# Performance work log

Measured on AMD Instinct MI355X. Metric: run time of the kernel, lower is better.

The kernel has to match this reference:

```python
import jax, jax.numpy as jnp
import numpy as np

BN_EPS = 1e-5

# Fixed shifted-difference kernels from the torch module (4,1,3,3)
_W1 = np.array([[[-1, 0, 0], [0, 1, 0], [0, 0, 0]],
                [[0, -1, 0], [0, 1, 0], [0, 0, 0]],
                [[0, 0, -1], [0, 1, 0], [0, 0, 0]],
                [[0, 0, 0], [-1, 1, 0], [0, 0, 0]]], dtype=np.float32).reshape(4, 1, 3, 3)
_W2 = np.ascontiguousarray(_W1[:, :, ::-1, ::-1])
SHIFTS = (1, 3)


def _conv(x, w, dilation=1):
    return jax.lax.conv_general_dilated(
        x, w, window_strides=(1, 1), padding='SAME',
        rhs_dilation=(dilation, dilation),
        dimension_numbers=('NCHW', 'OIHW', 'NCHW'))


def setup_inputs() -> dict:
    key = jax.random.key(0)
    ks = jax.random.split(key, 3)
    B, C, H, W = 4, 32, 512, 512
    cen = jax.random.normal(ks[0], (B, C, H, W), dtype=jnp.float32)
    w_conv = jax.random.normal(ks[1], (C, C, 3, 3), dtype=jnp.float32) * (1.0 / np.sqrt(9 * C))
    w_1x1 = jax.random.normal(ks[2], (1, C, 1, 1), dtype=jnp.float32) * (1.0 / np.sqrt(C))
    return {
        'cen': cen,
        'w_conv': w_conv,
        'bn_gamma': jnp.ones((C,), jnp.float32),
        'bn_beta': jnp.zeros((C,), jnp.float32),
        'bn_mean': jnp.zeros((C,), jnp.float32),
        'bn_var': jnp.ones((C,), jnp.float32),
        'w_1x1': w_1x1,
        'b_1x1': jnp.zeros((1,), jnp.float32),
    }


def reference(cen, w_conv, bn_gamma, bn_beta, bn_mean, bn_var, w_1x1, b_1x1):
    k1 = jnp.asarray(_W1)
    k2 = jnp.asarray(_W2)

    # down_conv: BaseConv(C->C, k3, s1) = Conv(no bias) + BN(eval) + SiLU, then 1x1 conv C->1
    x = _conv(cen, w_conv)
    inv = bn_gamma / jnp.sqrt(bn_var + BN_EPS)
    x = x * inv[None, :, None, None] + (bn_beta - bn_mean * inv)[None, :, None, None]
    x = jax.nn.silu(x)
    x = _conv(x, w_1x1) + b_1x1[None, :, None, None]  # [B,1,H,W]

    # circ_shift per dilation: fixed diff convs, product, min over 4 directions
    outs = []
    for s in SHIFTS:
        o1 = _conv(x, k1, dilation=s)  # [B,4,H,W]
        o2 = _conv(x, k2, dilation=s)
        outs.append(jnp.min(o1 * o2, axis=1, keepdims=True))  # [B,1,H,W]
    outs = jnp.stack(outs, axis=-1)  # [B,1,H,W,n_shifts]

    att = (jnp.max(outs, axis=-1) + jnp.mean(outs, axis=-1)) * 0.5
    att = jax.nn.sigmoid(jax.nn.relu(att))  # [B,1,H,W]
    return cen * att
```

## Files before the change

kernel.cpp:

```cpp
#include <hip/hip_runtime.h>
#include <hip/hip_bf16.h>
#include <math.h>

typedef __attribute__((ext_vector_type(8))) short bf16x8;
typedef __attribute__((ext_vector_type(4))) float f32x4;

#define HH 512
#define WW 512
#define CC 32

__device__ __forceinline__ unsigned short f2bf(float f) {
    unsigned u = __float_as_uint(f);
    u = (u + 0x7fffu + ((u >> 16) & 1u)) >> 16;
    return (unsigned short)u;
}

__global__ __launch_bounds__(256) void prepack(const float* __restrict__ wconv,
                                               unsigned short* __restrict__ wbuf) {
    int e = blockIdx.x * 256 + threadIdx.x;
    if (e < 9216) {
        int co  = e / 288;
        int rem = e - co * 288;
        int ci  = rem / 9;
        int t   = rem - ci * 9;
        wbuf[((t * 4 + (ci >> 3)) * 32 + co) * 8 + (ci & 7)] = f2bf(wconv[e]);
    }
}

__global__ __launch_bounds__(256) void conv_fused(
    const float* __restrict__ cen, const unsigned short* __restrict__ wbuf,
    const float* __restrict__ gamma, const float* __restrict__ beta,
    const float* __restrict__ mean, const float* __restrict__ var,
    const float* __restrict__ w1x1, const float* __restrict__ b1x1,
    float* __restrict__ xout)
{
    __shared__ unsigned short sIn[18 * 40 * 32];

    const int tid = threadIdx.x;
    const int b  = blockIdx.z;
    const int i0 = blockIdx.y << 4;
    const int j0 = blockIdx.x << 5;

    for (int e = tid; e < 2880; e += 256) {
        int r   = e / 160;
        int rem = e - r * 160;
        int cp  = rem & 15;
        int q   = rem >> 4;
        int gy  = i0 - 1 + r;
        int gx0 = j0 - 4 + 4 * q;
        f32x4 v0 = {0.f, 0.f, 0.f, 0.f}, v1 = {0.f, 0.f, 0.f, 0.f};
        if ((unsigned)gy < HH && (unsigned)gx0 < (WW - 3)) {
            const float* p = cen + (((long)(b * CC + 2 * cp) * HH + gy) * WW + gx0);
            v0 = *(const f32x4*)p;
            v1 = *(const f32x4*)(p + (long)HH * WW);
        }
        const int spb = r * 40 + 4 * q;
#pragma unroll
        for (int p2 = 0; p2 < 4; ++p2) {
            int sp = spb + p2;
            unsigned pk = (unsigned)f2bf(v0[p2]) | ((unsigned)f2bf(v1[p2]) << 16);
            int off = sp * 32 + ((((cp >> 2) ^ (sp & 3)) << 3) | ((cp & 3) << 1));
            *(unsigned*)&sIn[off] = pk;
        }
    }

    const int lane = tid & 63;
    const int wv   = tid >> 6;
    const int l15  = lane & 15;
    const int h    = lane >> 4;

    bf16x8 Bf[9][2];
#pragma unroll
    for (int t = 0; t < 9; ++t)
#pragma unroll
        for (int n = 0; n < 2; ++n)
            Bf[t][n] = *(const bf16x8*)&wbuf[((t * 4 + h) * 32 + n * 16 + l15) * 8];

    const float iv0 = gamma[l15]      / sqrtf(var[l15]      + 1e-5f);
    const float iv1 = gamma[l15 + 16] / sqrtf(var[l15 + 16] + 1e-5f);
    const float bb0 = beta[l15]      - mean[l15]      * iv0;
    const float bb1 = beta[l15 + 16] - mean[l15 + 16] * iv1;
    const float wa0 = w1x1[l15], wa1 = w1x1[l15 + 16];
    const float bias = b1x1[0];

    __syncthreads();

#pragma unroll
    for (int mt = 0; mt < 8; ++mt) {
        const int iloc = wv * 4 + (mt >> 1);
        const int jg   = mt & 1;
        const int xb   = jg * 16 + l15;
        f32x4 acc0 = {0.f, 0.f, 0.f, 0.f};
        f32x4 acc1 = {0.f, 0.f, 0.f, 0.f};
#pragma unroll
        for (int t = 0; t < 9; ++t) {
            const int sp = (iloc + t / 3) * 40 + xb + t % 3 + 3;
            bf16x8 A = *(const bf16x8*)&sIn[sp * 32 + ((h ^ (sp & 3)) << 3)];
            acc0 = __builtin_amdgcn_mfma_f32_16x16x32_bf16(A, Bf[t][0], acc0, 0, 0, 0);
            acc1 = __builtin_amdgcn_mfma_f32_16x16x32_bf16(A, Bf[t][1], acc1, 0, 0, 0);
        }
        float v[4];
#pragma unroll
        for (int r = 0; r < 4; ++r) {
            float y0 = acc0[r] * iv0 + bb0;
            float y1 = acc1[r] * iv1 + bb1;
            float s0 = y0 / (1.f + __expf(-y0));
            float s1 = y1 / (1.f + __expf(-y1));
            v[r] = wa0 * s0 + wa1 * s1;
        }
#pragma unroll
        for (int m = 1; m <= 8; m <<= 1) {
#pragma unroll
            for (int r = 0; r < 4; ++r)
                v[r] += __shfl_xor(v[r], m, 64);
        }
        if (l15 == 0) {
            const int i = i0 + iloc;
            const int j = j0 + jg * 16 + 4 * h;
            f32x4 o = {v[0] + bias, v[1] + bias, v[2] + bias, v[3] + bias};
            *(f32x4*)&xout[((long)b * HH + i) * WW + j] = o;
        }
    }
}

__global__ __launch_bounds__(256) void att_mul(
    const float* __restrict__ xin, const float* __restrict__ cen,
    float* __restrict__ out)
{
    __shared__ float xs[8 * 520];
    const int tid = threadIdx.x;
    const int b   = blockIdx.x >> 8;
    const int ip  = blockIdx.x & 255;
    const int gy0 = 2 * ip - 3;
    const float* xp = xin + (long)b * HH * WW;

    for (int e = tid; e < 1040; e += 256) {
        int r  = e / 130;
        int q  = e - r * 130;
        int gy = gy0 + r;
        int gx0 = 4 * q - 4;
        f32x4 v = {0.f, 0.f, 0.f, 0.f};
        if ((unsigned)gy < HH && (unsigned)gx0 < (WW - 3))
            v = *(const f32x4*)&xp[gy * WW + gx0];
        *(f32x4*)&xs[r * 520 + 4 * q] = v;
    }
    __syncthreads();

    const int jq = tid & 127;
    const int il = tid >> 7;
    const int i  = 2 * ip + il;
    const int j  = jq << 2;

    float w3m[12], w1m[12], wc0[12], w1p[12], w3p[12];
#pragma unroll
    for (int k = 0; k < 3; ++k) {
        f32x4 a;
        a = *(const f32x4*)&xs[(il + 0) * 520 + 4 * (jq + k)];
        w3m[4*k] = a.x; w3m[4*k+1] = a.y; w3m[4*k+2] = a.z; w3m[4*k+3] = a.w;
        a = *(const f32x4*)&xs[(il + 2) * 520 + 4 * (jq + k)];
        w1m[4*k] = a.x; w1m[4*k+1] = a.y; w1m[4*k+2] = a.z; w1m[4*k+3] = a.w;
        a = *(const f32x4*)&xs[(il + 3) * 520 + 4 * (jq + k)];
        wc0[4*k] = a.x; wc0[4*k+1] = a.y; wc0[4*k+2] = a.z; wc0[4*k+3] = a.w;
        a = *(const f32x4*)&xs[(il + 4) * 520 + 4 * (jq + k)];
        w1p[4*k] = a.x; w1p[4*k+1] = a.y; w1p[4*k+2] = a.z; w1p[4*k+3] = a.w;
        a = *(const f32x4*)&xs[(il + 6) * 520 + 4 * (jq + k)];
        w3p[4*k] = a.x; w3p[4*k+1] = a.y; w3p[4*k+2] = a.z; w3p[4*k+3] = a.w;
    }

    float att[4];
#pragma unroll
    for (int p = 0; p < 4; ++p) {
        const float c = wc0[p + 4];
        float d0 = (c - w1m[p + 3]) * (c - w1p[p + 5]);
        float d1 = (c - w1m[p + 4]) * (c - w1p[p + 4]);
        float d2 = (c - w1m[p + 5]) * (c - w1p[p + 3]);
        float d3 = (c - wc0[p + 3]) * (c - wc0[p + 5]);
        float o0 = fminf(fminf(d0, d1), fminf(d2, d3));
        d0 = (c - w3m[p + 1]) * (c - w3p[p + 7]);
        d1 = (c - w3m[p + 4]) * (c - w3p[p + 4]);
        d2 = (c - w3m[p + 7]) * (c - w3p[p + 1]);
        d3 = (c - wc0[p + 1]) * (c - wc0[p + 7]);
        float o1 = fminf(fminf(d0, d1), fminf(d2, d3));
        float a = 0.5f * (fmaxf(o0, o1) + 0.5f * (o0 + o1));
        a = a > 0.f ? a : 0.f;
        att[p] = 1.f / (1.f + __expf(-a));
    }

    const long rowoff = ((long)b * CC * HH + i) * WW + j;
#pragma unroll 8
    for (int c = 0; c < CC; ++c) {
        const long off = rowoff + (long)c * HH * WW;
        f32x4 v = *(const f32x4*)&cen[off];
        v.x *= att[0]; v.y *= att[1]; v.z *= att[2]; v.w *= att[3];
        *(f32x4*)&out[off] = v;
    }
}

extern "C" void kernel_launch(void* const* d_in, const int* in_sizes, int n_in,
                              void* d_out, int out_size, void* d_ws, size_t ws_size,
                              hipStream_t stream) {
    const float* cen   = (const float*)d_in[0];
    const float* wconv = (const float*)d_in[1];
    const float* gamma = (const float*)d_in[2];
    const float* beta  = (const float*)d_in[3];
    const float* mean  = (const float*)d_in[4];
    const float* var   = (const float*)d_in[5];
    const float* w1x1  = (const float*)d_in[6];
    const float* b1x1  = (const float*)d_in[7];
    float* xbuf = (float*)d_ws;
    unsigned short* wbuf = (unsigned short*)((char*)d_ws + (4l << 20));
    float* outp = (float*)d_out;

    prepack<<<dim3(36), 256, 0, stream>>>(wconv, wbuf);
    conv_fused<<<dim3(16, 32, 4), 256, 0, stream>>>(
        cen, wbuf, gamma, beta, mean, var, w1x1, b1x1, xbuf);
    att_mul<<<dim3(1024), 256, 0, stream>>>(xbuf, cen, outp);
}
```

Baseline: 316.4 us.

## Pre-transpose input to bf16 NHWC and split attention compute from apply

A new kernel converts the fp32 NCHW input into a bf16 NHWC copy, staged in the output buffer. The conv kernel then loads contiguous 16-byte channel vectors per pixel instead of gathering strided planes and converting in-kernel. The attention step is split into a kernel that writes a per-pixel attention map and a flat, fully coalesced elementwise multiply kernel. This adds an extra read of the input, a 64MB bf16 write and read, and two extra launches in exchange for better access patterns.

```diff
diff --git a/kernel.cpp b/kernel.cpp
--- a/kernel.cpp
+++ b/kernel.cpp
@@ -27,8 +27,39 @@
     }
 }
 
+__global__ __launch_bounds__(256) void to_nhwc(const float* __restrict__ cen,
+                                               unsigned short* __restrict__ nhwc) {
+    __shared__ float xs[32 * 132];
+    const int tid = threadIdx.x;
+    const int b  = blockIdx.z;
+    const int y  = blockIdx.y;
+    const int x0 = blockIdx.x << 7;
+
+#pragma unroll
+    for (int it = 0; it < 4; ++it) {
+        int e  = tid + (it << 8);
+        int ch = e >> 5;
+        int q  = e & 31;
+        f32x4 v = *(const f32x4*)&cen[(((long)(b * CC + ch) * HH + y) * WW) + x0 + 4 * q];
+        *(f32x4*)&xs[ch * 132 + 4 * q] = v;
+    }
+    __syncthreads();
+
+#pragma unroll
+    for (int it = 0; it < 2; ++it) {
+        int e  = tid + (it << 8);
+        int px = e >> 2;
+        int k  = e & 3;
+        unsigned short o[8];
+#pragma unroll
+        for (int i = 0; i < 8; ++i)
+            o[i] = f2bf(xs[(8 * k + i) * 132 + px]);
+        *(bf16x8*)&nhwc[(((long)(b * HH) + y) * WW + x0 + px) * 32 + 8 * k] = *(bf16x8*)o;
+    }
+}
+
 __global__ __launch_bounds__(256) void conv_fused(
-    const float* __restrict__ cen, const unsigned short* __restrict__ wbuf,
+    const unsigned short* __restrict__ nhwc, const unsigned short* __restrict__ wbuf,
     const float* __restrict__ gamma, const float* __restrict__ beta,
     const float* __restrict__ mean, const float* __restrict__ var,
     const float* __restrict__ w1x1, const float* __restrict__ b1x1,
@@ -42,26 +73,16 @@
     const int j0 = blockIdx.x << 5;
 
     for (int e = tid; e < 2880; e += 256) {
-        int r   = e / 160;
-        int rem = e - r * 160;
-        int cp  = rem & 15;
-        int q   = rem >> 4;
-        int gy  = i0 - 1 + r;
-        int gx0 = j0 - 4 + 4 * q;
-        f32x4 v0 = {0.f, 0.f, 0.f, 0.f}, v1 = {0.f, 0.f, 0.f, 0.f};
-        if ((unsigned)gy < HH && (unsigned)gx0 < (WW - 3)) {
-            const float* p = cen + (((long)(b * CC + 2 * cp) * HH + gy) * WW + gx0);
-            v0 = *(const f32x4*)p;
-            v1 = *(const f32x4*)(p + (long)HH * WW);
-        }
-        const int spb = r * 40 + 4 * q;
-#pragma unroll
-        for (int p2 = 0; p2 < 4; ++p2) {
-            int sp = spb + p2;
-            unsigned pk = (unsigned)f2bf(v0[p2]) | ((unsigned)f2bf(v1[p2]) << 16);
-            int off = sp * 32 + ((((cp >> 2) ^ (sp & 3)) << 3) | ((cp & 3) << 1));
-            *(unsigned*)&sIn[off] = pk;
-        }
+        int sp = e >> 2;
+        int k  = e & 3;
+        int r  = sp / 40;
+        int px = sp - r * 40;
+        int gy = i0 - 1 + r;
+        int gx = j0 - 4 + px;
+        bf16x8 v = {0, 0, 0, 0, 0, 0, 0, 0};
+        if ((unsigned)gy < HH && (unsigned)gx < WW)
+            v = *(const bf16x8*)&nhwc[(((long)(b * HH) + gy) * WW + gx) * 32 + 8 * k];
+        *(bf16x8*)&sIn[sp * 32 + ((k ^ (sp & 3)) << 3)] = v;
     }
 
     const int lane = tid & 63;
@@ -123,9 +144,8 @@
     }
 }
 
-__global__ __launch_bounds__(256) void att_mul(
-    const float* __restrict__ xin, const float* __restrict__ cen,
-    float* __restrict__ out)
+__global__ __launch_bounds__(256) void att_compute(
+    const float* __restrict__ xin, float* __restrict__ attbuf)
 {
     __shared__ float xs[8 * 520];
     const int tid = threadIdx.x;
@@ -167,7 +187,7 @@
         w3p[4*k] = a.x; w3p[4*k+1] = a.y; w3p[4*k+2] = a.z; w3p[4*k+3] = a.w;
     }
 
-    float att[4];
+    f32x4 attv;
 #pragma unroll
     for (int p = 0; p < 4; ++p) {
         const float c = wc0[p + 4];
@@ -183,16 +203,27 @@
         float o1 = fminf(fminf(d0, d1), fminf(d2, d3));
         float a = 0.5f * (fmaxf(o0, o1) + 0.5f * (o0 + o1));
         a = a > 0.f ? a : 0.f;
-        att[p] = 1.f / (1.f + __expf(-a));
-    }
-
-    const long rowoff = ((long)b * CC * HH + i) * WW + j;
-#pragma unroll 8
-    for (int c = 0; c < CC; ++c) {
-        const long off = rowoff + (long)c * HH * WW;
-        f32x4 v = *(const f32x4*)&cen[off];
-        v.x *= att[0]; v.y *= att[1]; v.z *= att[2]; v.w *= att[3];
-        *(f32x4*)&out[off] = v;
+        attv[p] = 1.f / (1.f + __expf(-a));
+    }
+    *(f32x4*)&attbuf[((long)b * HH + i) * WW + j] = attv;
+}
+
+__global__ __launch_bounds__(256) void att_apply(
+    const float* __restrict__ cen, const float* __restrict__ attbuf,
+    float* __restrict__ out)
+{
+    const f32x4* cv = (const f32x4*)cen;
+    const f32x4* av = (const f32x4*)attbuf;
+    f32x4* ov = (f32x4*)out;
+    const int t0 = blockIdx.x * 256 + threadIdx.x;
+#pragma unroll
+    for (int it = 0; it < 8; ++it) {
+        const int n = t0 + (it << 20);
+        const int aq = ((n >> 21) << 16) | (n & 65535);
+        f32x4 a = av[aq];
+        f32x4 c = cv[n];
+        c.x *= a.x; c.y *= a.y; c.z *= a.z; c.w *= a.w;
+        ov[n] = c;
     }
 }
 
@@ -207,12 +238,17 @@
     const float* var   = (const float*)d_in[5];
     const float* w1x1  = (const float*)d_in[6];
     const float* b1x1  = (const float*)d_in[7];
-    float* xbuf = (float*)d_ws;
-    unsigned short* wbuf = (unsigned short*)((char*)d_ws + (4l << 20));
+
+    float* xbuf   = (float*)d_ws;
+    float* attbuf = (float*)((char*)d_ws + (4l << 20));
+    unsigned short* wbuf = (unsigned short*)((char*)d_ws + (8l << 20));
+    unsigned short* nhwc = (unsigned short*)d_out;
     float* outp = (float*)d_out;
 
     prepack<<<dim3(36), 256, 0, stream>>>(wconv, wbuf);
+    to_nhwc<<<dim3(4, 512, 4), 256, 0, stream>>>(cen, nhwc);
     conv_fused<<<dim3(16, 32, 4), 256, 0, stream>>>(
-        cen, wbuf, gamma, beta, mean, var, w1x1, b1x1, xbuf);
-    att_mul<<<dim3(1024), 256, 0, stream>>>(xbuf, cen, outp);
-}
+        nhwc, wbuf, gamma, beta, mean, var, w1x1, b1x1, xbuf);
+    att_compute<<<dim3(1024), 256, 0, stream>>>(xbuf, attbuf);
+    att_apply<<<dim3(4096), 256, 0, stream>>>(cen, attbuf, outp);
+}
```

Result: slower. 332.8 us (+5.2%).
